# Performance work log

Hardware: AMD Instinct MI355X
Metric: run time of the kernel (lower is better)

Reference implementation:

```python
import jax, jax.numpy as jnp
import numpy as np

D_MODEL = 1024
N_HEADS = 16
HEAD_DIM = D_MODEL // N_HEADS


def setup_inputs() -> dict:
    key = jax.random.key(0)
    ks = jax.random.split(key, 5)
    B, T = 2, 2048
    x = jax.random.normal(ks[0], (B, T, D_MODEL), dtype=jnp.float32)
    s_in = 1.0 / np.sqrt(D_MODEL)
    W_qkv = jax.random.normal(ks[1], (D_MODEL, 3 * D_MODEL), dtype=jnp.float32) * s_in
    b_qkv = jnp.zeros((3 * D_MODEL,), dtype=jnp.float32)
    W_out = jax.random.normal(ks[2], (D_MODEL, D_MODEL), dtype=jnp.float32) * s_in
    b_out = jnp.zeros((D_MODEL,), dtype=jnp.float32)
    return {"x": x, "W_qkv": W_qkv, "b_qkv": b_qkv, "W_out": W_out, "b_out": b_out}


def reference(x, W_qkv, b_qkv, W_out, b_out):
    B, T, C = x.shape
    qkv = x @ W_qkv + b_qkv  # (B, T, 3C)
    q, k, v = jnp.split(qkv, 3, axis=-1)
    # (B, H, T, Dh)
    q = q.reshape(B, T, N_HEADS, HEAD_DIM).transpose(0, 2, 1, 3)
    k = k.reshape(B, T, N_HEADS, HEAD_DIM).transpose(0, 2, 1, 3)
    v = v.reshape(B, T, N_HEADS, HEAD_DIM).transpose(0, 2, 1, 3)
    scale = 1.0 / jnp.sqrt(jnp.asarray(HEAD_DIM, dtype=x.dtype))
    scores = jnp.einsum('bhqd,bhkd->bhqk', q, k) * scale  # (B, H, T, T)
    causal = jnp.tril(jnp.ones((T, T), dtype=bool))
    scores = jnp.where(causal[None, None], scores, jnp.asarray(-jnp.inf, dtype=scores.dtype))
    attn = jax.nn.softmax(scores, axis=-1)
    out = jnp.einsum('bhqk,bhkd->bhqd', attn, v)  # (B, H, T, Dh)
    out = out.transpose(0, 2, 1, 3).reshape(B, T, C)
    return out @ W_out + b_out
```

## Files before the change

kernel.cpp:

```cpp
#include <hip/hip_runtime.h>
#include <hip/hip_bf16.h>
#include <stdint.h>

typedef __bf16 bf16;
typedef __bf16 bf16x4 __attribute__((ext_vector_type(4)));
typedef __bf16 bf16x8 __attribute__((ext_vector_type(8)));
typedef float  f32x4  __attribute__((ext_vector_type(4)));

#define D_MODEL 1024
#define N_HEADS 16
#define HEAD_DIM 64
#define SEQ 2048
#define BATCH 2
#define LOG2E 1.4426950408889634f
#define NEG_SENT -3.0e4f
#define CAP 24.0f

__device__ __forceinline__ bf16x8 ld8(const bf16* p) { return *(const bf16x8*)p; }

__device__ __forceinline__ void async16(const bf16* g, bf16* l) {
  __builtin_amdgcn_global_load_lds(
      (const __attribute__((address_space(1))) void*)g,
      (__attribute__((address_space(3))) void*)l, 16, 0, 0);
}

__global__ __launch_bounds__(256)
void prep(const float* __restrict__ x, bf16* __restrict__ x16,
          const float* __restrict__ Wqkv, bf16* __restrict__ Wqkv_t,
          const float* __restrict__ Wout, bf16* __restrict__ Wout_t) {
  __shared__ float tile[32][33];
  const int blk = blockIdx.x, tid = threadIdx.x;
  if (blk < 4096) {
    int i = (blk * 256 + tid) * 4;
    float4 v = *(const float4*)&x[i];
    bf16 o[4] = {(bf16)v.x, (bf16)v.y, (bf16)v.z, (bf16)v.w};
    *(uint2*)&x16[i] = *(uint2*)o;
    return;
  }
  const float* in; bf16* out; int R, C, c0, r0;
  if (blk < 7168) {
    int b = blk - 4096;
    in = Wqkv; out = Wqkv_t; R = 1024; C = 3072;
    c0 = (b % 96) * 32; r0 = (b / 96) * 32;
  } else {
    int b = blk - 7168;
    in = Wout; out = Wout_t; R = 1024; C = 1024;
    c0 = (b % 32) * 32; r0 = (b / 32) * 32;
  }
  const int tx = tid & 31, ty = tid >> 5;
  #pragma unroll
  for (int i = 0; i < 32; i += 8)
    tile[ty + i][tx] = in[(size_t)(r0 + ty + i) * C + c0 + tx];
  __syncthreads();
  #pragma unroll
  for (int i = 0; i < 32; i += 8)
    out[(size_t)(c0 + ty + i) * R + r0 + tx] = (bf16)tile[tx][ty + i];
}

__global__ __launch_bounds__(256)
void gemm_bt(const bf16* __restrict__ A, const bf16* __restrict__ Bt,
             const float* __restrict__ bias, float* __restrict__ outf,
             bf16* __restrict__ Qp, bf16* __restrict__ Kp, bf16* __restrict__ Vtp,
             int N, int mode) {
  __shared__ __align__(16) bf16 shA[2][128 * 32];
  __shared__ __align__(16) bf16 shB[2][128 * 32];
  const int tid  = threadIdx.x;
  const int bm0  = blockIdx.y * 128, bn0 = blockIdx.x * 128;
  const int wave = tid >> 6, lane = tid & 63;
  const int quad = lane >> 4, l16 = lane & 15;
  const int wm = (wave >> 1) * 64, wn = (wave & 1) * 64;

  const int c_lo  = tid;
  const int row_lo = c_lo >> 2,  col_lo = (c_lo & 3) << 3;
  const int c_hi  = tid + 256;
  const int row_hi = c_hi >> 2,  col_hi = (c_hi & 3) << 3;
  const int cb_lo = (wave * 64) * 8;
  const int cb_hi = (256 + wave * 64) * 8;

  f32x4 acc[4][4];
  #pragma unroll
  for (int i = 0; i < 4; i++)
    #pragma unroll
    for (int j = 0; j < 4; j++)
      acc[i][j] = (f32x4){0.f, 0.f, 0.f, 0.f};

  for (int k0 = 0; k0 < 1024; k0 += 64) {
    #pragma unroll
    for (int kk = 0; kk < 2; kk++) {
      const int kb = k0 + kk * 32;
      async16(&A[(size_t)(bm0 + row_lo) * 1024 + kb + col_lo], &shA[kk][cb_lo]);
      async16(&A[(size_t)(bm0 + row_hi) * 1024 + kb + col_hi], &shA[kk][cb_hi]);
      async16(&Bt[(size_t)(bn0 + row_lo) * 1024 + kb + col_lo], &shB[kk][cb_lo]);
      async16(&Bt[(size_t)(bn0 + row_hi) * 1024 + kb + col_hi], &shB[kk][cb_hi]);
    }
    __syncthreads();
    #pragma unroll
    for (int kk = 0; kk < 2; kk++) {
      bf16x8 af[4], bg[4];
      #pragma unroll
      for (int i = 0; i < 4; i++)
        af[i] = ld8(&shA[kk][(wm + i * 16 + l16) * 32 + quad * 8]);
      #pragma unroll
      for (int j = 0; j < 4; j++)
        bg[j] = ld8(&shB[kk][(wn + j * 16 + l16) * 32 + quad * 8]);
      #pragma unroll
      for (int i = 0; i < 4; i++)
        #pragma unroll
        for (int j = 0; j < 4; j++)
          acc[i][j] = __builtin_amdgcn_mfma_f32_16x16x32_bf16(af[i], bg[j], acc[i][j], 0, 0, 0);
    }
    __syncthreads();
  }

  #pragma unroll
  for (int i = 0; i < 4; i++) {
    #pragma unroll
    for (int j = 0; j < 4; j++) {
      int gn = bn0 + wn + j * 16 + l16;
      float bv = bias[gn];
      int gm0 = bm0 + wm + i * 16 + quad * 4;
      if (mode == 1) {
        #pragma unroll
        for (int r = 0; r < 4; r++)
          outf[(size_t)(gm0 + r) * N + gn] = acc[i][j][r] + bv;
      } else {
        int which = gn >> 10, rem = gn & 1023;
        int h = rem >> 6, d = rem & 63;
        int b = gm0 >> 11, t0 = gm0 & 2047;
        int bh = b * N_HEADS + h;
        if (which == 2) {
          bf16x4 vv = {(bf16)(acc[i][j][0] + bv), (bf16)(acc[i][j][1] + bv),
                       (bf16)(acc[i][j][2] + bv), (bf16)(acc[i][j][3] + bv)};
          *(bf16x4*)&Vtp[((size_t)bh * 64 + d) * SEQ + t0] = vv;
        } else {
          bf16* dst = (which == 0) ? Qp : Kp;
          #pragma unroll
          for (int r = 0; r < 4; r++)
            dst[((size_t)bh * SEQ + t0 + r) * 64 + d] = (bf16)(acc[i][j][r] + bv);
        }
      }
    }
  }
}

__global__ __launch_bounds__(256)
void gemm_out(const bf16* __restrict__ A, const bf16* __restrict__ Bt,
              const float* __restrict__ bias, float* __restrict__ outf) {
  __shared__ __align__(16) bf16 shA[64 * 32];
  __shared__ __align__(16) bf16 shB[128 * 32];
  const int tid  = threadIdx.x;
  const int bm0  = blockIdx.y * 64, bn0 = blockIdx.x * 128;
  const int wave = tid >> 6, lane = tid & 63;
  const int quad = lane >> 4, l16 = lane & 15;
  const int wn = wave * 32;

  f32x4 acc[4][2];
  #pragma unroll
  for (int i = 0; i < 4; i++)
    #pragma unroll
    for (int j = 0; j < 2; j++)
      acc[i][j] = (f32x4){0.f, 0.f, 0.f, 0.f};

  const int srow = tid >> 2, scol = (tid & 3) << 3;
  for (int k0 = 0; k0 < 1024; k0 += 32) {
    async16(&A[(size_t)(bm0 + srow) * 1024 + k0 + scol], &shA[tid * 8]);
    async16(&Bt[(size_t)(bn0 + srow) * 1024 + k0 + scol], &shB[tid * 8]);
    async16(&Bt[(size_t)(bn0 + 64 + srow) * 1024 + k0 + scol], &shB[(256 + tid) * 8]);
    __syncthreads();
    bf16x8 af[4], bg[2];
    #pragma unroll
    for (int i = 0; i < 4; i++)
      af[i] = ld8(&shA[(i * 16 + l16) * 32 + quad * 8]);
    #pragma unroll
    for (int j = 0; j < 2; j++)
      bg[j] = ld8(&shB[(wn + j * 16 + l16) * 32 + quad * 8]);
    #pragma unroll
    for (int i = 0; i < 4; i++)
      #pragma unroll
      for (int j = 0; j < 2; j++)
        acc[i][j] = __builtin_amdgcn_mfma_f32_16x16x32_bf16(af[i], bg[j], acc[i][j], 0, 0, 0);
    __syncthreads();
  }

  #pragma unroll
  for (int i = 0; i < 4; i++) {
    #pragma unroll
    for (int j = 0; j < 2; j++) {
      int gn = bn0 + wn + j * 16 + l16;
      float bv = bias[gn];
      int gm0 = bm0 + i * 16 + quad * 4;
      #pragma unroll
      for (int r = 0; r < 4; r++)
        outf[(size_t)(gm0 + r) * D_MODEL + gn] = acc[i][j][r] + bv;
    }
  }
}

__global__ __launch_bounds__(256)
void attn_k(const bf16* __restrict__ Qp, const bf16* __restrict__ Kp,
            const bf16* __restrict__ Vtp, bf16* __restrict__ Obuf) {
  __shared__ __align__(16) bf16 shK[2][128 * 64];
  __shared__ __align__(16) bf16 shV[2][64 * 128];
  __shared__ __align__(16) bf16 shPT[4][16 * 72];
  const int tid  = threadIdx.x;
  const int wave = tid >> 6, lane = tid & 63;
  const int quad = lane >> 4, l16 = lane & 15;
  const int bx = blockIdx.x;
  const int g = bx >> 5;
  const int qb = (g < 8) ? g : 23 - g;
  const int bh = bx & 31;
  const int qw0 = qb * 128 + wave * 32;

  const bf16* Qbh = Qp  + (size_t)bh * SEQ * 64;
  const bf16* Kbh = Kp  + (size_t)bh * SEQ * 64;
  const bf16* Vbh = Vtp + (size_t)bh * 64 * SEQ;

  bf16x8 aQ[2][2];
  #pragma unroll
  for (int g2 = 0; g2 < 2; g2++)
    #pragma unroll
    for (int p = 0; p < 2; p++)
      aQ[g2][p] = ld8(&Qbh[(size_t)(qw0 + g2 * 16 + l16) * 64 + p * 32 + quad * 8]);

  f32x4 o0[4], o1[4];
  #pragma unroll
  for (int j = 0; j < 4; j++) { o0[j] = (f32x4){0.f,0.f,0.f,0.f}; o1[j] = (f32x4){0.f,0.f,0.f,0.f}; }
  f32x4 lacc0 = (f32x4){0.f,0.f,0.f,0.f}, lacc1 = (f32x4){0.f,0.f,0.f,0.f};
  const int qlane0 = qw0 + l16, qlane1 = qw0 + 16 + l16;
  const int xq = l16 & 7;

  const float SC = 0.125f * LOG2E;
  bf16* PT = shPT[wave];

  #pragma unroll
  for (int s2 = 0; s2 < 4; s2++) {
    int id = tid + s2 * 256;
    int kr = id >> 3, kc = id & 7;
    async16(&Kbh[(size_t)kr * 64 + (kc ^ (kr & 7)) * 8], &shK[0][id * 8]);
  }
  #pragma unroll
  for (int s2 = 0; s2 < 4; s2++) {
    int id = tid + s2 * 256;
    int vd = id >> 4, vc = id & 15;
    int svc = (vc & 8) | ((vc & 7) ^ (vd & 7));
    async16(&Vbh[(size_t)vd * SEQ + svc * 8], &shV[0][id * 8]);
  }
  __syncthreads();

  const int NT = qb + 1;
  int cur = 0;
  for (int kt = 0; kt < NT; kt++) {
    if (kt + 1 < NT) {
      const int kb1 = (kt + 1) * 128;
      #pragma unroll
      for (int s2 = 0; s2 < 4; s2++) {
        int id = tid + s2 * 256;
        int kr = id >> 3, kc = id & 7;
        async16(&Kbh[(size_t)(kb1 + kr) * 64 + (kc ^ (kr & 7)) * 8],
                &shK[cur ^ 1][id * 8]);
      }
      #pragma unroll
      for (int s2 = 0; s2 < 4; s2++) {
        int id = tid + s2 * 256;
        int vd = id >> 4, vc = id & 15;
        int svc = (vc & 8) | ((vc & 7) ^ (vd & 7));
        async16(&Vbh[(size_t)vd * SEQ + kb1 + svc * 8], &shV[cur ^ 1][id * 8]);
      }
    }

    const bf16* Kb = shK[cur];
    const bf16* Vb = shV[cur];

    #pragma unroll
    for (int h = 0; h < 2; h++) {
      const int hb = kt * 128 + h * 64;
      if (hb > qw0 + 31) continue;

      f32x4 st0[4], st1[4];
      __builtin_amdgcn_s_setprio(1);
      #pragma unroll
      for (int c = 0; c < 4; c++) {
        int kr0 = h * 64 + c * 16 + l16;
        bf16x8 kf0 = ld8(&Kb[kr0 * 64 + ((quad    ) ^ xq) * 8]);
        bf16x8 kf1 = ld8(&Kb[kr0 * 64 + ((quad + 4) ^ xq) * 8]);
        f32x4 a0 = (f32x4){0.f,0.f,0.f,0.f};
        a0 = __builtin_amdgcn_mfma_f32_16x16x32_bf16(kf0, aQ[0][0], a0, 0, 0, 0);
        a0 = __builtin_amdgcn_mfma_f32_16x16x32_bf16(kf1, aQ[0][1], a0, 0, 0, 0);
        f32x4 a1 = (f32x4){0.f,0.f,0.f,0.f};
        a1 = __builtin_amdgcn_mfma_f32_16x16x32_bf16(kf0, aQ[1][0], a1, 0, 0, 0);
        a1 = __builtin_amdgcn_mfma_f32_16x16x32_bf16(kf1, aQ[1][1], a1, 0, 0, 0);
        st0[c] = a0; st1[c] = a1;
      }
      __builtin_amdgcn_s_setprio(0);

      if (hb + 63 > qw0) {
        #pragma unroll
        for (int c = 0; c < 4; c++)
          #pragma unroll
          for (int r = 0; r < 4; r++) {
            int key = hb + c * 16 + quad * 4 + r;
            if (key > qlane0) st0[c][r] = NEG_SENT;
            if (key > qlane1) st1[c][r] = NEG_SENT;
          }
      }

      #pragma unroll
      for (int c = 0; c < 4; c++) {
        #pragma unroll
        for (int r = 0; r < 4; r++) {
          st0[c][r] = exp2f(__builtin_fmaf(st0[c][r], SC, -CAP));
          st1[c][r] = exp2f(__builtin_fmaf(st1[c][r], SC, -CAP));
        }
        lacc0 += st0[c]; lacc1 += st1[c];
      }

      #pragma unroll
      for (int c = 0; c < 4; c++) {
        bf16x4 p0 = {(bf16)st0[c][0], (bf16)st0[c][1], (bf16)st0[c][2], (bf16)st0[c][3]};
        *(bf16x4*)&PT[l16 * 72 + c * 16 + quad * 4] = p0;
      }
      asm volatile("s_waitcnt lgkmcnt(0)" ::: "memory");
      bf16x8 bP00 = ld8(&PT[l16 * 72 + quad * 8]);
      bf16x8 bP01 = ld8(&PT[l16 * 72 + 32 + quad * 8]);

      #pragma unroll
      for (int c = 0; c < 4; c++) {
        bf16x4 p1 = {(bf16)st1[c][0], (bf16)st1[c][1], (bf16)st1[c][2], (bf16)st1[c][3]};
        *(bf16x4*)&PT[l16 * 72 + c * 16 + quad * 4] = p1;
      }
      asm volatile("s_waitcnt lgkmcnt(0)" ::: "memory");
      bf16x8 bP10 = ld8(&PT[l16 * 72 + quad * 8]);
      bf16x8 bP11 = ld8(&PT[l16 * 72 + 32 + quad * 8]);

      __builtin_amdgcn_s_setprio(1);
      #pragma unroll
      for (int j = 0; j < 4; j++) {
        int d = j * 16 + l16;
        bf16x8 v0 = ld8(&Vb[d * 128 + ((h * 8) | ((quad    ) ^ xq)) * 8]);
        bf16x8 v1 = ld8(&Vb[d * 128 + ((h * 8) | ((quad + 4) ^ xq)) * 8]);
        o0[j] = __builtin_amdgcn_mfma_f32_16x16x32_bf16(v0, bP00, o0[j], 0, 0, 0);
        o0[j] = __builtin_amdgcn_mfma_f32_16x16x32_bf16(v1, bP01, o0[j], 0, 0, 0);
        o1[j] = __builtin_amdgcn_mfma_f32_16x16x32_bf16(v0, bP10, o1[j], 0, 0, 0);
        o1[j] = __builtin_amdgcn_mfma_f32_16x16x32_bf16(v1, bP11, o1[j], 0, 0, 0);
      }
      __builtin_amdgcn_s_setprio(0);
    }

    __syncthreads();
    cur ^= 1;
  }

  const int b = bh >> 4, h = bh & 15;
  {
    float lr0 = (lacc0[0] + lacc0[1]) + (lacc0[2] + lacc0[3]);
    lr0 += __shfl_xor(lr0, 16, 64);
    lr0 += __shfl_xor(lr0, 32, 64);
    float lr1 = (lacc1[0] + lacc1[1]) + (lacc1[2] + lacc1[3]);
    lr1 += __shfl_xor(lr1, 16, 64);
    lr1 += __shfl_xor(lr1, 32, 64);
    float inv0 = 1.0f / lr0, inv1 = 1.0f / lr1;
    size_t base0 = ((size_t)(b * SEQ + qw0 + l16)) * D_MODEL + h * 64;
    size_t base1 = ((size_t)(b * SEQ + qw0 + 16 + l16)) * D_MODEL + h * 64;
    #pragma unroll
    for (int j = 0; j < 4; j++) {
      bf16x4 ov0 = {(bf16)(o0[j][0] * inv0), (bf16)(o0[j][1] * inv0),
                    (bf16)(o0[j][2] * inv0), (bf16)(o0[j][3] * inv0)};
      bf16x4 ov1 = {(bf16)(o1[j][0] * inv1), (bf16)(o1[j][1] * inv1),
                    (bf16)(o1[j][2] * inv1), (bf16)(o1[j][3] * inv1)};
      *(bf16x4*)&Obuf[base0 + j * 16 + quad * 4] = ov0;
      *(bf16x4*)&Obuf[base1 + j * 16 + quad * 4] = ov1;
    }
  }
}

extern "C" void kernel_launch(void* const* d_in, const int* in_sizes, int n_in,
                              void* d_out, int out_size, void* d_ws, size_t ws_size,
                              hipStream_t stream) {
  const float* x    = (const float*)d_in[0];
  const float* Wqkv = (const float*)d_in[1];
  const float* bqkv = (const float*)d_in[2];
  const float* Wout = (const float*)d_in[3];
  const float* bout = (const float*)d_in[4];
  float* out = (float*)d_out;

  char* ws = (char*)d_ws;
  bf16* x16    = (bf16*)(ws);
  bf16* Wqkv_t = (bf16*)(ws + 8388608);
  bf16* Wout_t = (bf16*)(ws + 14680064);
  bf16* Qp     = (bf16*)(ws + 16777216);
  bf16* Kp     = (bf16*)(ws + 25165824);
  bf16* Vtp    = (bf16*)(ws + 33554432);
  bf16* Obuf   = x16;

  prep<<<8192, 256, 0, stream>>>(x, x16, Wqkv, Wqkv_t, Wout, Wout_t);

  gemm_bt<<<dim3(3072 / 128, 4096 / 128), 256, 0, stream>>>(
      x16, Wqkv_t, bqkv, nullptr, Qp, Kp, Vtp, 3072, 0);

  attn_k<<<dim3(512), 256, 0, stream>>>(Qp, Kp, Vtp, Obuf);

  gemm_out<<<dim3(1024 / 128, 4096 / 64), 256, 0, stream>>>(
      Obuf, Wout_t, bout, out);
}
```

Before: 188.1 us.

## Shrink attention blocks to 64 queries with 2 waves and 64-key tiles

Reworks the attention kernel so each block handles 64 query rows with two waves instead of 128 rows with four, and streams K/V in 64-key tiles instead of 128. The grid doubles to 1024 blocks, and the causal load-balancing pairing of query blocks is dropped in favour of linear ordering. The goal is more, smaller blocks for better occupancy and finer causal skipping. The cost is more K/V reloads from global memory per query row and more barriers per key.

```diff
diff --git a/kernel.cpp b/kernel.cpp
--- a/kernel.cpp
+++ b/kernel.cpp
@@ -196,20 +196,19 @@
   }
 }
 
-__global__ __launch_bounds__(256)
+__global__ __launch_bounds__(128)
 void attn_k(const bf16* __restrict__ Qp, const bf16* __restrict__ Kp,
             const bf16* __restrict__ Vtp, bf16* __restrict__ Obuf) {
-  __shared__ __align__(16) bf16 shK[2][128 * 64];
-  __shared__ __align__(16) bf16 shV[2][64 * 128];
-  __shared__ __align__(16) bf16 shPT[4][16 * 72];
+  __shared__ __align__(16) bf16 shK[2][64 * 64];
+  __shared__ __align__(16) bf16 shV[2][64 * 64];
+  __shared__ __align__(16) bf16 shPT[2][16 * 72];
   const int tid  = threadIdx.x;
   const int wave = tid >> 6, lane = tid & 63;
   const int quad = lane >> 4, l16 = lane & 15;
   const int bx = blockIdx.x;
-  const int g = bx >> 5;
-  const int qb = (g < 8) ? g : 23 - g;
+  const int qb = bx >> 5;
   const int bh = bx & 31;
-  const int qw0 = qb * 128 + wave * 32;
+  const int qw0 = qb * 64 + wave * 32;
 
   const bf16* Qbh = Qp  + (size_t)bh * SEQ * 64;
   const bf16* Kbh = Kp  + (size_t)bh * SEQ * 64;
@@ -233,54 +232,40 @@
   bf16* PT = shPT[wave];
 
   #pragma unroll
-  for (int s2 = 0; s2 < 4; s2++) {
-    int id = tid + s2 * 256;
+  for (int i = 0; i < 4; i++) {
+    int id = tid + i * 128;
     int kr = id >> 3, kc = id & 7;
     async16(&Kbh[(size_t)kr * 64 + (kc ^ (kr & 7)) * 8], &shK[0][id * 8]);
-  }
-  #pragma unroll
-  for (int s2 = 0; s2 < 4; s2++) {
-    int id = tid + s2 * 256;
-    int vd = id >> 4, vc = id & 15;
-    int svc = (vc & 8) | ((vc & 7) ^ (vd & 7));
-    async16(&Vbh[(size_t)vd * SEQ + svc * 8], &shV[0][id * 8]);
+    async16(&Vbh[(size_t)kr * SEQ + (kc ^ (kr & 7)) * 8], &shV[0][id * 8]);
   }
   __syncthreads();
 
-  const int NT = qb + 1;
+  const int NS = qb + 1;
   int cur = 0;
-  for (int kt = 0; kt < NT; kt++) {
-    if (kt + 1 < NT) {
-      const int kb1 = (kt + 1) * 128;
-      #pragma unroll
-      for (int s2 = 0; s2 < 4; s2++) {
-        int id = tid + s2 * 256;
+  for (int s = 0; s < NS; s++) {
+    if (s + 1 < NS) {
+      const int kb1 = (s + 1) * 64;
+      #pragma unroll
+      for (int i = 0; i < 4; i++) {
+        int id = tid + i * 128;
         int kr = id >> 3, kc = id & 7;
         async16(&Kbh[(size_t)(kb1 + kr) * 64 + (kc ^ (kr & 7)) * 8],
                 &shK[cur ^ 1][id * 8]);
-      }
-      #pragma unroll
-      for (int s2 = 0; s2 < 4; s2++) {
-        int id = tid + s2 * 256;
-        int vd = id >> 4, vc = id & 15;
-        int svc = (vc & 8) | ((vc & 7) ^ (vd & 7));
-        async16(&Vbh[(size_t)vd * SEQ + kb1 + svc * 8], &shV[cur ^ 1][id * 8]);
-      }
-    }
-
-    const bf16* Kb = shK[cur];
-    const bf16* Vb = shV[cur];
-
-    #pragma unroll
-    for (int h = 0; h < 2; h++) {
-      const int hb = kt * 128 + h * 64;
-      if (hb > qw0 + 31) continue;
+        async16(&Vbh[(size_t)kr * SEQ + kb1 + (kc ^ (kr & 7)) * 8],
+                &shV[cur ^ 1][id * 8]);
+      }
+    }
+
+    const int hb = s * 64;
+    if (hb <= qw0 + 31) {
+      const bf16* Kb = shK[cur];
+      const bf16* Vb = shV[cur];
 
       f32x4 st0[4], st1[4];
       __builtin_amdgcn_s_setprio(1);
       #pragma unroll
       for (int c = 0; c < 4; c++) {
-        int kr0 = h * 64 + c * 16 + l16;
+        int kr0 = c * 16 + l16;
         bf16x8 kf0 = ld8(&Kb[kr0 * 64 + ((quad    ) ^ xq) * 8]);
         bf16x8 kf1 = ld8(&Kb[kr0 * 64 + ((quad + 4) ^ xq) * 8]);
         f32x4 a0 = (f32x4){0.f,0.f,0.f,0.f};
@@ -336,8 +321,8 @@
       #pragma unroll
       for (int j = 0; j < 4; j++) {
         int d = j * 16 + l16;
-        bf16x8 v0 = ld8(&Vb[d * 128 + ((h * 8) | ((quad    ) ^ xq)) * 8]);
-        bf16x8 v1 = ld8(&Vb[d * 128 + ((h * 8) | ((quad + 4) ^ xq)) * 8]);
+        bf16x8 v0 = ld8(&Vb[d * 64 + ((quad    ) ^ xq) * 8]);
+        bf16x8 v1 = ld8(&Vb[d * 64 + ((quad + 4) ^ xq) * 8]);
         o0[j] = __builtin_amdgcn_mfma_f32_16x16x32_bf16(v0, bP00, o0[j], 0, 0, 0);
         o0[j] = __builtin_amdgcn_mfma_f32_16x16x32_bf16(v1, bP01, o0[j], 0, 0, 0);
         o1[j] = __builtin_amdgcn_mfma_f32_16x16x32_bf16(v0, bP10, o1[j], 0, 0, 0);
@@ -397,7 +382,7 @@
   gemm_bt<<<dim3(3072 / 128, 4096 / 128), 256, 0, stream>>>(
       x16, Wqkv_t, bqkv, nullptr, Qp, Kp, Vtp, 3072, 0);
 
-  attn_k<<<dim3(512), 256, 0, stream>>>(Qp, Kp, Vtp, Obuf);
+  attn_k<<<dim3(1024), 128, 0, stream>>>(Qp, Kp, Vtp, Obuf);
 
   gemm_out<<<dim3(1024 / 128, 4096 / 64), 256, 0, stream>>>(
       Obuf, Wout_t, bout, out);
```

After: 206.6 us. 1.1x slower.
